# Performance work log

Measured on AMD Instinct MI355X. Metric: run time of the kernel, lower is better.

The kernel has to match this reference:

```python
import jax, jax.numpy as jnp
import numpy as np
import math

B, H, N, D = 8, 8, 2048, 64
CLIP = 10.0
NEG_INF = 1.0e10

def setup_inputs() -> dict:
    key = jax.random.key(0)
    kq, kk, kv, km = jax.random.split(key, 4)
    Q = jax.random.normal(kq, (B, H, N, D), dtype=jnp.float32)
    K = jax.random.normal(kk, (B, H, N, D), dtype=jnp.float32)
    V = jax.random.normal(kv, (B, H, N, D), dtype=jnp.float32)
    mask = jax.random.randint(km, (B, N, 1), 0, 2).astype(jnp.bool_)
    return {"Q": Q, "K": K, "V": V, "mask": mask}

def reference(Q, K, V, mask):
    scale = math.sqrt(Q.shape[-1])
    # logits: (B, H, Nq, Nk)
    logits = jnp.einsum("bhqd,bhkd->bhqk", Q, K) / scale
    logits = CLIP * jnp.tanh(logits)
    # mask (B, N, 1) -> broadcast over heads and query dim along key axis
    m = mask[:, None, None, :, 0]  # (B, 1, 1, Nk)
    logits = jnp.where(m, -NEG_INF, logits)
    probs = jax.nn.softmax(logits, axis=-1)
    return jnp.einsum("bhqk,bhkd->bhqd", probs, V)
```

## Files before the change

### kernel.cpp

```cpp
#include <hip/hip_runtime.h>

typedef __attribute__((ext_vector_type(8))) short short8;
typedef __attribute__((ext_vector_type(8))) _Float16 half8;
typedef __attribute__((ext_vector_type(2))) __fp16 fp16x2;
typedef __attribute__((ext_vector_type(2))) unsigned int uint2v;
typedef __attribute__((ext_vector_type(16))) float f32x16;
typedef __attribute__((ext_vector_type(4))) float f32x4;
typedef __attribute__((ext_vector_type(4))) unsigned short u16x4;
typedef __attribute__((ext_vector_type(8))) unsigned short u16x8;
typedef unsigned int u32;
typedef unsigned short u16;

#define B_ 8
#define H_ 8
#define N_ 2048
#define D_ 64
#define PSTR 72
#define TSTR 66
#define ELEMS 8388608
#define WS_NEED ((48ull << 20) + 4096ull)

static __device__ inline u16 bfhi(float x) {
  u32 u = __float_as_uint(x);
  return (u16)((u + 0x7FFFu + ((u >> 16) & 1u)) >> 16);
}
static __device__ inline float bf2f(u16 h) { return __uint_as_float((u32)h << 16); }
static __device__ inline u16 h2u(_Float16 h) { union { _Float16 f; u16 u; } c; c.f = h; return c.u; }

static __device__ __forceinline__ u32 pkrtz_u32(float a, float b) {
  union { fp16x2 h; u32 u; } c;
  c.h = __builtin_amdgcn_cvt_pkrtz(a, b);
  return c.u;
}

template <bool TAIL>
static __device__ __forceinline__ float pnum(float s, int key, int rem) {
  float z  = __builtin_amdgcn_exp2f(fabsf(s) * -0.36067376022224087f);
  float nu = (s >= 0.f) ? z : 1.f;
  float e  = nu * __builtin_amdgcn_rcpf(1.f + z) * -28.853900817779268f;
  if (TAIL) e = (key < rem) ? e : -16384.f;
  return __builtin_amdgcn_exp2f(e);
}

static __device__ __forceinline__ half8 pack_frag(
    float qa, float qb, float qc, float qd,
    float qe, float qf, float qg, float qh) {
  u32 E0 = pkrtz_u32(qa, qb);
  u32 E1 = pkrtz_u32(qc, qd);
  u32 O0 = pkrtz_u32(qe, qf);
  u32 O1 = pkrtz_u32(qg, qh);
  uint2v w0 = __builtin_amdgcn_permlane32_swap(E0, O0, false, false);
  uint2v w1 = __builtin_amdgcn_permlane32_swap(E1, O1, false, false);
  union { u32 u[4]; half8 v; } c;
  c.u[0] = w0[0]; c.u[1] = w1[0]; c.u[2] = w0[1]; c.u[3] = w1[1];
  return c.v;
}

struct FragSum { half8 f; float s; };

template <bool TAIL>
static __device__ __forceinline__ FragSum pack8(
    f32x16 S, int rbase, int koff, int rem) {
#define KEYI(i) ((((rbase) + (i)) & 3) + 8 * (((rbase) + (i)) >> 2) + (koff))
  float pA = pnum<TAIL>(S[rbase + 0], KEYI(0), rem);
  float pB = pnum<TAIL>(S[rbase + 1], KEYI(1), rem);
  float pC = pnum<TAIL>(S[rbase + 2], KEYI(2), rem);
  float pD = pnum<TAIL>(S[rbase + 3], KEYI(3), rem);
  float pE = pnum<TAIL>(S[rbase + 4], KEYI(4), rem);
  float pF = pnum<TAIL>(S[rbase + 5], KEYI(5), rem);
  float pG = pnum<TAIL>(S[rbase + 6], KEYI(6), rem);
  float pH = pnum<TAIL>(S[rbase + 7], KEYI(7), rem);
#undef KEYI
  FragSum o;
  o.f = pack_frag(pA, pB, pC, pD, pE, pF, pG, pH);
  o.s = ((pA + pB) + (pC + pD)) + ((pE + pF) + (pG + pH));
  return o;
}

__global__ __launch_bounds__(256) void conv_kv3(
    const float* __restrict__ K, const float* __restrict__ V,
    const int* __restrict__ maskg,
    u16* __restrict__ Khi, u16* __restrict__ Klo, u16* __restrict__ VThi,
    int* __restrict__ cnt) {
  const int kt = blockIdx.x, bh = blockIdx.y, b = bh >> 3, tid = threadIdx.x;
  const int lane = tid & 63, wv = tid >> 6;
  __shared__ float sT[64 * TSTR];
  __shared__ int sIdx[64];
  __shared__ int wsum[4];
  const int n0 = tid * 8;
  u32 bits = 0; int c = 0;
#pragma unroll
  for (int i = 0; i < 8; ++i)
    if (maskg[b * N_ + n0 + i] == 0) { bits |= (1u << i); ++c; }
  int inc = c;
#pragma unroll
  for (int off = 1; off < 64; off <<= 1) {
    int v = __shfl_up(inc, off);
    if (lane >= off) inc += v;
  }
  if (lane == 63) wsum[wv] = inc;
  if (tid < 64) sIdx[tid] = -1;
  __syncthreads();
  const int cntb = wsum[0] + wsum[1] + wsum[2] + wsum[3];
  int o = inc - c;
#pragma unroll
  for (int k2 = 0; k2 < 4; ++k2) if (k2 < wv) o += wsum[k2];
  const int k0 = kt * 64;
#pragma unroll
  for (int i = 0; i < 8; ++i)
    if (bits & (1u << i)) {
      if (o >= k0 && o < k0 + 64) sIdx[o - k0] = n0 + i;
      ++o;
    }
  if (kt == 0 && (bh & 7) == 0 && tid == 0) cnt[b] = cntb;
  __syncthreads();
  const int nt = (cntb + 63) >> 6;
  if (kt >= nt) return;

  const size_t ibh = (size_t)bh * N_ * D_;
  const size_t okb = ibh + (size_t)kt * 64 * D_;
#pragma unroll
  for (int cc = 0; cc < 2; ++cc) {
    const int ci = tid + cc * 256, row = ci >> 3, seg = ci & 7;
    const int n = sIdx[row];
    f32x4 a, b2, va, vb2;
    if (n >= 0) {
      const float* kp = K + ibh + (size_t)n * D_ + seg * 8;
      a  = *(const f32x4*)kp;
      b2 = *(const f32x4*)(kp + 4);
      const float* vp = V + ibh + (size_t)n * D_ + seg * 8;
      va  = *(const f32x4*)vp;
      vb2 = *(const f32x4*)(vp + 4);
    } else {
#pragma unroll
      for (int j = 0; j < 4; ++j) { a[j] = 0.f; b2[j] = 0.f; va[j] = 0.f; vb2[j] = 0.f; }
    }
    u16x8 h, l;
#pragma unroll
    for (int j = 0; j < 4; ++j) {
      _Float16 h0 = (_Float16)a[j];
      h[j] = h2u(h0); l[j] = h2u((_Float16)(a[j] - (float)h0));
      _Float16 h1 = (_Float16)b2[j];
      h[j + 4] = h2u(h1); l[j + 4] = h2u((_Float16)(b2[j] - (float)h1));
    }
    *(u16x8*)&Khi[okb + row * D_ + seg * 8] = h;
    *(u16x8*)&Klo[okb + row * D_ + seg * 8] = l;
    *(f32x4*)&sT[row * TSTR + seg * 8]     = va;
    *(f32x4*)&sT[row * TSTR + seg * 8 + 4] = vb2;
  }
  __syncthreads();
  const int key0 = (tid & 15) * 4, d0 = (tid >> 4) * 4;
  f32x4 r0 = *(const f32x4*)&sT[(key0 + 0) * TSTR + d0];
  f32x4 r1 = *(const f32x4*)&sT[(key0 + 1) * TSTR + d0];
  f32x4 r2 = *(const f32x4*)&sT[(key0 + 2) * TSTR + d0];
  f32x4 r3 = *(const f32x4*)&sT[(key0 + 3) * TSTR + d0];
  const size_t ob = (size_t)bh * D_ * N_ + (size_t)kt * 64 + key0;
#pragma unroll
  for (int j = 0; j < 4; ++j) {
    u16x4 ov;
    ov[0] = h2u((_Float16)r0[j]); ov[1] = h2u((_Float16)r1[j]);
    ov[2] = h2u((_Float16)r2[j]); ov[3] = h2u((_Float16)r3[j]);
    *(u16x4*)&VThi[ob + (size_t)(d0 + j) * N_] = ov;
  }
}

__global__ __launch_bounds__(256, 4) void attn_mfma7(
    const float* __restrict__ Qg,
    const u16* __restrict__ Khi, const u16* __restrict__ Klo,
    const u16* __restrict__ VThi,
    const int* __restrict__ cnt, float* __restrict__ Og)
{
  const int blk = blockIdx.x;
  const int xcd = blk & 7, slot = blk >> 3;
  const int bh = ((slot >> 4) << 3) | xcd;
  const int qtile = slot & 15;
  const int b = bh >> 3;
  const int tid = threadIdx.x, w = tid >> 6, lane = tid & 63;
  const int l32 = lane & 31, hl = lane >> 5;
  const int cntb = cnt[b];
  const int nt = (cntb + 63) >> 6;
  const bool partial = (cntb & 63) != 0;

  __shared__ short sKh[64 * PSTR], sKl[64 * PSTR];
  __shared__ short sVh[64 * PSTR];

  half8 qfh[4], qfl[4];
  {
    const float* qp = Qg + ((size_t)bh * N_ + qtile * 128 + w * 32 + l32) * D_ + hl * 8;
#pragma unroll
    for (int s = 0; s < 4; ++s) {
      f32x4 a = *(const f32x4*)(qp + s * 16);
      f32x4 c = *(const f32x4*)(qp + s * 16 + 4);
#pragma unroll
      for (int j = 0; j < 4; ++j) {
        _Float16 h0 = (_Float16)a[j];
        qfh[s][j] = h0; qfl[s][j] = (_Float16)(a[j] - (float)h0);
        _Float16 h1 = (_Float16)c[j];
        qfh[s][j + 4] = h1; qfl[s][j + 4] = (_Float16)(c[j] - (float)h1);
      }
    }
  }

  f32x16 accO0, accO1;
#pragma unroll
  for (int i = 0; i < 16; ++i) { accO0[i] = 0.f; accO1[i] = 0.f; }
  float dsum = 0.f;

  const size_t kvb = (size_t)bh * N_ * D_;

  short8 rKh[2], rKl[2], rVh[2];
#pragma unroll
  for (int cc = 0; cc < 2; ++cc) {
    const int ci = tid + cc * 256, row = ci >> 3, seg = ci & 7;
    rKh[cc] = *(const short8*)&Khi[kvb + (size_t)row * D_ + seg * 8];
    rKl[cc] = *(const short8*)&Klo[kvb + (size_t)row * D_ + seg * 8];
    rVh[cc] = *(const short8*)&VThi[kvb + (size_t)row * N_ + seg * 8];
  }

  for (int kt = 0; kt < nt; ++kt) {
    __syncthreads();

#pragma unroll
    for (int cc = 0; cc < 2; ++cc) {
      const int ci = tid + cc * 256, row = ci >> 3, seg = ci & 7;
      const int lofs = row * PSTR + seg * 8;
      *(short8*)&sKh[lofs] = rKh[cc];
      *(short8*)&sKl[lofs] = rKl[cc];
      *(short8*)&sVh[lofs] = rVh[cc];
    }
    __syncthreads();

    f32x16 S0, S1;
#pragma unroll
    for (int i = 0; i < 16; ++i) { S0[i] = 0.f; S1[i] = 0.f; }
    __builtin_amdgcn_s_setprio(1);
#pragma unroll
    for (int s = 0; s < 4; ++s) {
      const int o0 = l32 * PSTR + s * 16 + hl * 8;
      half8 kfh = *(const half8*)&sKh[o0];
      half8 kfl = *(const half8*)&sKl[o0];
      S0 = __builtin_amdgcn_mfma_f32_32x32x16_f16(kfh, qfh[s], S0, 0, 0, 0);
      S0 = __builtin_amdgcn_mfma_f32_32x32x16_f16(kfl, qfh[s], S0, 0, 0, 0);
      S0 = __builtin_amdgcn_mfma_f32_32x32x16_f16(kfh, qfl[s], S0, 0, 0, 0);
      const int o1 = (32 + l32) * PSTR + s * 16 + hl * 8;
      half8 kgh = *(const half8*)&sKh[o1];
      half8 kgl = *(const half8*)&sKl[o1];
      S1 = __builtin_amdgcn_mfma_f32_32x32x16_f16(kgh, qfh[s], S1, 0, 0, 0);
      S1 = __builtin_amdgcn_mfma_f32_32x32x16_f16(kgl, qfh[s], S1, 0, 0, 0);
      S1 = __builtin_amdgcn_mfma_f32_32x32x16_f16(kgh, qfl[s], S1, 0, 0, 0);
    }
    __builtin_amdgcn_s_setprio(0);

    FragSum fs0, fs1, fs2, fs3;
    if (partial && kt == nt - 1) {
      const int rem = cntb - kt * 64 - 4 * hl;
      fs0 = pack8<true>(S0, 0, 0, rem);
      fs1 = pack8<true>(S0, 8, 0, rem);
      fs2 = pack8<true>(S1, 0, 32, rem);
      fs3 = pack8<true>(S1, 8, 32, rem);
    } else {
      fs0 = pack8<false>(S0, 0, 0, 0);
      fs1 = pack8<false>(S0, 8, 0, 0);
      fs2 = pack8<false>(S1, 0, 32, 0);
      fs3 = pack8<false>(S1, 8, 32, 0);
    }
    dsum += (fs0.s + fs1.s) + (fs2.s + fs3.s);

    {
      const int k0n = (kt + 1 < nt ? kt + 1 : kt) * 64;
#pragma unroll
      for (int cc = 0; cc < 2; ++cc) {
        const int ci = tid + cc * 256, row = ci >> 3, seg = ci & 7;
        rKh[cc] = *(const short8*)&Khi[kvb + (size_t)(k0n + row) * D_ + seg * 8];
        rKl[cc] = *(const short8*)&Klo[kvb + (size_t)(k0n + row) * D_ + seg * 8];
        rVh[cc] = *(const short8*)&VThi[kvb + (size_t)row * N_ + k0n + seg * 8];
      }
    }

    __builtin_amdgcn_s_setprio(1);
#define PV_STEP(sI, PF)                                                        \
    {                                                                          \
      const int o0 = l32 * PSTR + (sI) * 16 + hl * 8;                          \
      half8 v0 = *(const half8*)&sVh[o0];                                      \
      accO0 = __builtin_amdgcn_mfma_f32_32x32x16_f16((PF), v0, accO0, 0, 0, 0);\
      const int o1 = (32 + l32) * PSTR + (sI) * 16 + hl * 8;                   \
      half8 v1 = *(const half8*)&sVh[o1];                                      \
      accO1 = __builtin_amdgcn_mfma_f32_32x32x16_f16((PF), v1, accO1, 0, 0, 0);\
    }
    PV_STEP(0, fs0.f)
    PV_STEP(1, fs1.f)
    PV_STEP(2, fs2.f)
    PV_STEP(3, fs3.f)
#undef PV_STEP
    __builtin_amdgcn_s_setprio(0);
  }

  float dtot = dsum + __shfl_xor(dsum, 32);
  const size_t obase = (size_t)bh * N_ + qtile * 128 + w * 32;
#pragma unroll
  for (int r = 0; r < 16; ++r) {
    const int row = (r & 3) + 8 * (r >> 2) + 4 * hl;
    float den = __shfl(dtot, row);
    float inv = (den > 0.f) ? (1.f / den) : 0.f;
    Og[(obase + row) * D_ + l32]      = accO0[r] * inv;
    Og[(obase + row) * D_ + 32 + l32] = accO1[r] * inv;
  }
}

__global__ __launch_bounds__(256, 3) void attn_mfma(
    const float* __restrict__ Qg, const float* __restrict__ Kg,
    const float* __restrict__ Vg, const int* __restrict__ maskg,
    float* __restrict__ Og)
{
  const int qtile = blockIdx.x;
  const int bh    = blockIdx.y;
  const int b     = bh >> 3;
  const int tid   = threadIdx.x;
  const int w     = tid >> 6;
  const int lane  = tid & 63;
  const int l32   = lane & 31;
  const int hl    = lane >> 5;
  const int qh    = w >> 1;
  const int kh    = w & 1;

  __shared__ short sKh[64 * PSTR], sKl[64 * PSTR];
  __shared__ short sVh[64 * PSTR], sVl[64 * PSTR];
  __shared__ short sP [64 * PSTR];
  __shared__ float sM[64];

  short8 qfh[4], qfl[4];
  {
    const float* qp = Qg + ((size_t)bh * N_ + qtile * 64 + qh * 32 + l32) * D_ + hl * 8;
#pragma unroll
    for (int s = 0; s < 4; ++s) {
      f32x4 a = *(const f32x4*)(qp + s * 16);
      f32x4 c = *(const f32x4*)(qp + s * 16 + 4);
#pragma unroll
      for (int j = 0; j < 4; ++j) {
        u16 h0 = bfhi(a[j]);
        qfh[s][j] = (short)h0;
        qfl[s][j] = (short)bfhi(a[j] - bf2f(h0));
        u16 h1 = bfhi(c[j]);
        qfh[s][j + 4] = (short)h1;
        qfl[s][j + 4] = (short)bfhi(c[j] - bf2f(h1));
      }
    }
  }
  short8 ones;
#pragma unroll
  for (int j = 0; j < 8; ++j) ones[j] = (short)((l32 == 0) ? 0x3F80 : 0);
  f32x16 accO, accD;
#pragma unroll
  for (int i = 0; i < 16; ++i) { accO[i] = 0.f; accD[i] = 0.f; }
  const size_t kvbase = (size_t)bh * N_ * D_;

  for (int kt = 0; kt < N_ / 64; ++kt) {
    const int k0 = kt * 64;
    __syncthreads();
    {
      const int row = tid >> 2, seg = tid & 3;
      const float* kp = Kg + kvbase + (size_t)(k0 + row) * D_ + seg * 16;
      short8 h0, h1, l0, l1;
#pragma unroll
      for (int i2 = 0; i2 < 2; ++i2) {
        f32x4 t0 = *(const f32x4*)(kp + i2 * 8);
        f32x4 t1 = *(const f32x4*)(kp + i2 * 8 + 4);
#pragma unroll
        for (int j = 0; j < 4; ++j) {
          u16 ha = bfhi(t0[j]); u16 la = bfhi(t0[j] - bf2f(ha));
          u16 hb = bfhi(t1[j]); u16 lb = bfhi(t1[j] - bf2f(hb));
          if (i2 == 0) { h0[j]=(short)ha; l0[j]=(short)la; h0[j+4]=(short)hb; l0[j+4]=(short)lb; }
          else         { h1[j]=(short)ha; l1[j]=(short)la; h1[j+4]=(short)hb; l1[j+4]=(short)lb; }
        }
      }
      *(short8*)&sKh[row * PSTR + seg * 16]     = h0;
      *(short8*)&sKh[row * PSTR + seg * 16 + 8] = h1;
      *(short8*)&sKl[row * PSTR + seg * 16]     = l0;
      *(short8*)&sKl[row * PSTR + seg * 16 + 8] = l1;
    }
    {
      const float* vp = Vg + kvbase + (size_t)(k0 + w * 16) * D_ + lane;
      float vv[16];
#pragma unroll
      for (int kk = 0; kk < 16; ++kk) vv[kk] = vp[(size_t)kk * D_];
      short8 h0, h1, l0, l1;
#pragma unroll
      for (int kk = 0; kk < 8; ++kk) {
        u16 ha = bfhi(vv[kk]);     h0[kk]=(short)ha; l0[kk]=(short)bfhi(vv[kk]-bf2f(ha));
        u16 hb = bfhi(vv[kk + 8]); h1[kk]=(short)hb; l1[kk]=(short)bfhi(vv[kk+8]-bf2f(hb));
      }
      *(short8*)&sVh[lane * PSTR + w * 16]     = h0;
      *(short8*)&sVh[lane * PSTR + w * 16 + 8] = h1;
      *(short8*)&sVl[lane * PSTR + w * 16]     = l0;
      *(short8*)&sVl[lane * PSTR + w * 16 + 8] = l1;
    }
    if (tid < 64) sM[tid] = maskg[b * N_ + k0 + tid] ? 0.f : 1.f;
    __syncthreads();

    f32x16 S;
#pragma unroll
    for (int i = 0; i < 16; ++i) S[i] = 0.f;
#pragma unroll
    for (int s = 0; s < 4; ++s) {
      const int off = (kh * 32 + l32) * PSTR + s * 16 + hl * 8;
      short8 kfh = *(const short8*)&sKh[off];
      short8 kfl = *(const short8*)&sKl[off];
      S = __builtin_amdgcn_mfma_f32_32x32x16_bf16(qfh[s], kfh, S, 0, 0, 0);
      S = __builtin_amdgcn_mfma_f32_32x32x16_bf16(qfl[s], kfh, S, 0, 0, 0);
      S = __builtin_amdgcn_mfma_f32_32x32x16_bf16(qfh[s], kfl, S, 0, 0, 0);
    }
    const float pm = sM[kh * 32 + l32];
#pragma unroll
    for (int r = 0; r < 16; ++r) {
      float x  = S[r] * 0.125f;
      float ax = fminf(fabsf(x), 30.f);
      float z  = __builtin_amdgcn_exp2f(ax * -2.8853900817779268f);
      float nu = (x >= 0.f) ? z : 1.f;
      float e  = nu * __builtin_amdgcn_rcpf(1.f + z) * -28.853900817779268f;
      float p  = __builtin_amdgcn_exp2f(e) * pm;
      const int row = qh * 32 + (r & 3) + 8 * (r >> 2) + 4 * hl;
      sP[row * PSTR + kh * 32 + l32] = (short)bfhi(p);
    }
    __syncthreads();
#pragma unroll
    for (int s = 0; s < 4; ++s) {
      short8 pf  = *(const short8*)&sP[(qh * 32 + l32) * PSTR + s * 16 + hl * 8];
      const int voff = (kh * 32 + l32) * PSTR + s * 16 + hl * 8;
      short8 vfh = *(const short8*)&sVh[voff];
      short8 vfl = *(const short8*)&sVl[voff];
      accO = __builtin_amdgcn_mfma_f32_32x32x16_bf16(pf, vfh, accO, 0, 0, 0);
      accO = __builtin_amdgcn_mfma_f32_32x32x16_bf16(pf, vfl, accO, 0, 0, 0);
      accD = __builtin_amdgcn_mfma_f32_32x32x16_bf16(pf, ones, accD, 0, 0, 0);
    }
  }
  const size_t obase = (size_t)bh * N_ + qtile * 64 + qh * 32;
#pragma unroll
  for (int r = 0; r < 16; ++r) {
    float den = __shfl(accD[r], lane & 32);
    float inv = (den > 0.f) ? (1.f / den) : 0.f;
    const int row = (r & 3) + 8 * (r >> 2) + 4 * hl;
    Og[(obase + row) * D_ + kh * 32 + l32] = accO[r] * inv;
  }
}

extern "C" void kernel_launch(void* const* d_in, const int* in_sizes, int n_in,
                              void* d_out, int out_size, void* d_ws, size_t ws_size,
                              hipStream_t stream) {
  const float* Q = (const float*)d_in[0];
  const float* K = (const float*)d_in[1];
  const float* V = (const float*)d_in[2];
  const int* mask = (const int*)d_in[3];
  float* out = (float*)d_out;
  dim3 block(256);
  if (ws_size >= (size_t)WS_NEED) {
    u16* wsp  = (u16*)d_ws;
    u16* Khi  = wsp;
    u16* Klo  = wsp + ELEMS;
    u16* VThi = wsp + 2 * (size_t)ELEMS;
    int* cntp = (int*)(wsp + 3 * (size_t)ELEMS);
    conv_kv3<<<dim3(32, 64), block, 0, stream>>>(K, V, mask, Khi, Klo, VThi, cntp);
    attn_mfma7<<<dim3(1024), block, 0, stream>>>(Q, Khi, Klo, VThi, cntp, out);
  } else {
    attn_mfma<<<dim3(32, 64), block, 0, stream>>>(Q, K, V, mask, out);
  }
}
```

Before: 257.1 us.

## Simplify tanh-softmax numerator, use nontemporal loads/stores, pointer-increment prefetch

Replaces the sign-split sigmoid form of the clipped-tanh exponent with a single exp2 and reciprocal, dropping the abs, select and multiply. Marks K/V/Q reads and output writes as nontemporal so single-use streams are meant to avoid polluting cache. The prefetch of the next K/V tile now uses incrementing pointers and is skipped on the last iteration, replacing a redundant reload with per-iteration index arithmetic. The new exponent form can overflow exp2 for large positive logits; rcp of infinity gives zero, so the result likely stays correct.

```diff
diff --git a/kernel.cpp b/kernel.cpp
--- a/kernel.cpp
+++ b/kernel.cpp
@@ -35,9 +35,8 @@
 
 template <bool TAIL>
 static __device__ __forceinline__ float pnum(float s, int key, int rem) {
-  float z  = __builtin_amdgcn_exp2f(fabsf(s) * -0.36067376022224087f);
-  float nu = (s >= 0.f) ? z : 1.f;
-  float e  = nu * __builtin_amdgcn_rcpf(1.f + z) * -28.853900817779268f;
+  float t = __builtin_amdgcn_exp2f(s * 0.36067376022224087f);
+  float e = __builtin_amdgcn_rcpf(1.f + t) * -28.853900817779268f;
   if (TAIL) e = (key < rem) ? e : -16384.f;
   return __builtin_amdgcn_exp2f(e);
 }
@@ -126,11 +125,11 @@
     f32x4 a, b2, va, vb2;
     if (n >= 0) {
       const float* kp = K + ibh + (size_t)n * D_ + seg * 8;
-      a  = *(const f32x4*)kp;
-      b2 = *(const f32x4*)(kp + 4);
+      a  = __builtin_nontemporal_load((const f32x4*)kp);
+      b2 = __builtin_nontemporal_load((const f32x4*)(kp + 4));
       const float* vp = V + ibh + (size_t)n * D_ + seg * 8;
-      va  = *(const f32x4*)vp;
-      vb2 = *(const f32x4*)(vp + 4);
+      va  = __builtin_nontemporal_load((const f32x4*)vp);
+      vb2 = __builtin_nontemporal_load((const f32x4*)(vp + 4));
     } else {
 #pragma unroll
       for (int j = 0; j < 4; ++j) { a[j] = 0.f; b2[j] = 0.f; va[j] = 0.f; vb2[j] = 0.f; }
@@ -164,7 +163,7 @@
   }
 }
 
-__global__ __launch_bounds__(256, 4) void attn_mfma7(
+__global__ __launch_bounds__(256, 4) void attn_mfma8(
     const float* __restrict__ Qg,
     const u16* __restrict__ Khi, const u16* __restrict__ Klo,
     const u16* __restrict__ VThi,
@@ -189,8 +188,8 @@
     const float* qp = Qg + ((size_t)bh * N_ + qtile * 128 + w * 32 + l32) * D_ + hl * 8;
 #pragma unroll
     for (int s = 0; s < 4; ++s) {
-      f32x4 a = *(const f32x4*)(qp + s * 16);
-      f32x4 c = *(const f32x4*)(qp + s * 16 + 4);
+      f32x4 a = __builtin_nontemporal_load((const f32x4*)(qp + s * 16));
+      f32x4 c = __builtin_nontemporal_load((const f32x4*)(qp + s * 16 + 4));
 #pragma unroll
       for (int j = 0; j < 4; ++j) {
         _Float16 h0 = (_Float16)a[j];
@@ -208,25 +207,25 @@
 
   const size_t kvb = (size_t)bh * N_ * D_;
 
+  const int prow = tid >> 3, pseg = tid & 7;
+  const u16* pKh = Khi + kvb + (size_t)prow * D_ + pseg * 8;
+  const u16* pKl = Klo + kvb + (size_t)prow * D_ + pseg * 8;
+  const u16* pV  = VThi + kvb + (size_t)prow * N_ + pseg * 8;
+
   short8 rKh[2], rKl[2], rVh[2];
-#pragma unroll
-  for (int cc = 0; cc < 2; ++cc) {
-    const int ci = tid + cc * 256, row = ci >> 3, seg = ci & 7;
-    rKh[cc] = *(const short8*)&Khi[kvb + (size_t)row * D_ + seg * 8];
-    rKl[cc] = *(const short8*)&Klo[kvb + (size_t)row * D_ + seg * 8];
-    rVh[cc] = *(const short8*)&VThi[kvb + (size_t)row * N_ + seg * 8];
-  }
+  rKh[0] = *(const short8*)pKh; rKh[1] = *(const short8*)(pKh + 32 * D_);
+  rKl[0] = *(const short8*)pKl; rKl[1] = *(const short8*)(pKl + 32 * D_);
+  rVh[0] = *(const short8*)pV;  rVh[1] = *(const short8*)(pV + 32 * N_);
+  pKh += 64 * D_; pKl += 64 * D_; pV += 64;
 
   for (int kt = 0; kt < nt; ++kt) {
     __syncthreads();
 
-#pragma unroll
-    for (int cc = 0; cc < 2; ++cc) {
-      const int ci = tid + cc * 256, row = ci >> 3, seg = ci & 7;
-      const int lofs = row * PSTR + seg * 8;
-      *(short8*)&sKh[lofs] = rKh[cc];
-      *(short8*)&sKl[lofs] = rKl[cc];
-      *(short8*)&sVh[lofs] = rVh[cc];
+    {
+      const int lofs = prow * PSTR + pseg * 8;
+      *(short8*)&sKh[lofs] = rKh[0]; *(short8*)&sKh[lofs + 32 * PSTR] = rKh[1];
+      *(short8*)&sKl[lofs] = rKl[0]; *(short8*)&sKl[lofs + 32 * PSTR] = rKl[1];
+      *(short8*)&sVh[lofs] = rVh[0]; *(short8*)&sVh[lofs + 32 * PSTR] = rVh[1];
     }
     __syncthreads();
 
@@ -266,15 +265,11 @@
     }
     dsum += (fs0.s + fs1.s) + (fs2.s + fs3.s);
 
-    {
-      const int k0n = (kt + 1 < nt ? kt + 1 : kt) * 64;
-#pragma unroll
-      for (int cc = 0; cc < 2; ++cc) {
-        const int ci = tid + cc * 256, row = ci >> 3, seg = ci & 7;
-        rKh[cc] = *(const short8*)&Khi[kvb + (size_t)(k0n + row) * D_ + seg * 8];
-        rKl[cc] = *(const short8*)&Klo[kvb + (size_t)(k0n + row) * D_ + seg * 8];
-        rVh[cc] = *(const short8*)&VThi[kvb + (size_t)row * N_ + k0n + seg * 8];
-      }
+    if (kt + 1 < nt) {
+      rKh[0] = *(const short8*)pKh; rKh[1] = *(const short8*)(pKh + 32 * D_);
+      rKl[0] = *(const short8*)pKl; rKl[1] = *(const short8*)(pKl + 32 * D_);
+      rVh[0] = *(const short8*)pV;  rVh[1] = *(const short8*)(pV + 32 * N_);
+      pKh += 64 * D_; pKl += 64 * D_; pV += 64;
     }
 
     __builtin_amdgcn_s_setprio(1);
@@ -302,8 +297,8 @@
     const int row = (r & 3) + 8 * (r >> 2) + 4 * hl;
     float den = __shfl(dtot, row);
     float inv = (den > 0.f) ? (1.f / den) : 0.f;
-    Og[(obase + row) * D_ + l32]      = accO0[r] * inv;
-    Og[(obase + row) * D_ + 32 + l32] = accO1[r] * inv;
+    __builtin_nontemporal_store(accO0[r] * inv, &Og[(obase + row) * D_ + l32]);
+    __builtin_nontemporal_store(accO1[r] * inv, &Og[(obase + row) * D_ + 32 + l32]);
   }
 }
 
@@ -459,7 +454,7 @@
     u16* VThi = wsp + 2 * (size_t)ELEMS;
     int* cntp = (int*)(wsp + 3 * (size_t)ELEMS);
     conv_kv3<<<dim3(32, 64), block, 0, stream>>>(K, V, mask, Khi, Klo, VThi, cntp);
-    attn_mfma7<<<dim3(1024), block, 0, stream>>>(Q, Khi, Klo, VThi, cntp, out);
+    attn_mfma8<<<dim3(1024), block, 0, stream>>>(Q, Khi, Klo, VThi, cntp, out);
   } else {
     attn_mfma<<<dim3(32, 64), block, 0, stream>>>(Q, K, V, mask, out);
   }
```

Measured after the change: 283.3 us. +10.2%, slower.
